# Kernel optimization log

Hardware: AMD Instinct MI355X
Metric: run time of the kernel (lower is better)

## Reference

```python
import jax, jax.numpy as jnp
import numpy as np

EPS = 0.5  # diffusion epsilon from init_kwargs

def setup_inputs() -> dict:
    key = jax.random.key(0)
    k = jax.random.split(key, 7)
    B, N0, N1, n = 1024, 32, 32, 64
    Mu0 = jax.random.normal(k[0], (N0, n), dtype=jnp.float32) * 2.0
    Mu1 = jax.random.normal(k[1], (N1, n), dtype=jnp.float32) * 2.0
    # diagonal covariances must be positive
    S0 = jax.random.uniform(k[2], (N0, n), dtype=jnp.float32, minval=0.1, maxval=1.0)
    S1 = jax.random.uniform(k[3], (N1, n), dtype=jnp.float32, minval=0.1, maxval=1.0)
    Lam = jax.random.uniform(k[4], (N0, N1), dtype=jnp.float32, minval=0.0, maxval=1.0)
    Lam = Lam / Lam.sum()  # transport plan sums to 1
    X = jax.random.normal(k[5], (B, n), dtype=jnp.float32)
    t = jnp.float32(0.3)
    return {"X": X, "Mu0": Mu0, "Mu1": Mu1, "S0": S0, "S1": S1, "Lam": Lam, "t": t}

def reference(X, Mu0, Mu1, S0, S1, Lam, t):
    eps2 = EPS * EPS
    S0e = S0[:, None, :]        # (N0,1,n)
    S1e = S1[None, :, :]        # (1,N1,n)
    Ds = jnp.sqrt(4.0 * S0e * S1e + EPS ** 4)
    Cs = 0.5 * (Ds - eps2)                       # (N0,N1,n)
    mu_t = (1.0 - t) * Mu0[:, None, :] + t * Mu1[None, :, :]  # (N0,N1,n)
    Sigma = (1.0 - t) ** 2 * S0e + t ** 2 * S1e + 2.0 * t * (1.0 - t) * (Cs + 0.5 * eps2)
    # St = Pt - Qt - eps^2 * t
    St = t * S1e + (1.0 - t) * Cs - ((1.0 - t) * S0e + t * Cs) - eps2 * t
    K = St / Sigma                               # (N0,N1,n)
    v = Mu1[None, :, :] - Mu0[:, None, :]        # (N0,N1,n)
    d = X[:, None, None, :] - mu_t               # (B,N0,N1,n)
    U = K * d + v                                # (B,N0,N1,n)
    # diag-Normal log_prob plus n/2*log(2pi) == -0.5*sum(d^2/Sigma + log Sigma)
    logw = -0.5 * jnp.sum(d * d / Sigma + jnp.log(Sigma), axis=-1)  # (B,N0,N1)
    W = jnp.exp(jnp.clip(logw, -50.0, 50.0)) * Lam                  # (B,N0,N1)
    num = jnp.einsum('bijn,bij->bn', U, W)       # (B,n)
    den = jnp.sum(W, axis=(1, 2))[:, None]       # (B,1)
    return num / den
```

## Files before the change

kernel.cpp:

```cpp
#include <hip/hip_runtime.h>
#include <math.h>

#define EPS2f 0.25f
#define EPS4f 0.0625f

__global__ __launch_bounds__(256) void precomp_kernel(
    const float* __restrict__ Mu0, const float* __restrict__ Mu1,
    const float* __restrict__ S0,  const float* __restrict__ S1,
    const float* __restrict__ tptr,
    float2* __restrict__ AB2, float2* __restrict__ KV2,
    float* __restrict__ C0)
{
    __shared__ float2 abS[4][67];
    __shared__ float2 kvS[4][64];

    const int tid = threadIdx.x;
    const int k   = tid & 63;
    const int ijl = tid >> 6;
    const int ij0 = blockIdx.x << 2;
    const int ij  = ij0 + ijl;
    const int i   = ij >> 5;
    const int j   = ij & 31;
    const float t   = *tptr;
    const float omt = 1.0f - t;

    const float s0 = S0[i * 64 + k];
    const float s1 = S1[j * 64 + k];
    const float m0 = Mu0[i * 64 + k];
    const float m1 = Mu1[j * 64 + k];

    const float ds  = sqrtf(4.0f * s0 * s1 + EPS4f);
    const float cs  = 0.5f * (ds - EPS2f);
    const float mt  = omt * m0 + t * m1;
    const float sig = omt * omt * s0 + t * t * s1
                    + 2.0f * t * omt * (cs + 0.5f * EPS2f);
    const float isig = 1.0f / sig;
    const float st = t * s1 - omt * s0 + (omt - t) * cs - EPS2f * t;
    const float kk = st * isig;
    const float v  = m1 - m0;

    abS[ijl][k] = make_float2(isig, 2.0f * mt * isig);
    kvS[ijl][k] = make_float2(kk, v - kk * mt);

    float c = mt * mt * isig + __logf(sig);
    #pragma unroll
    for (int off = 32; off >= 1; off >>= 1)
        c += __shfl_xor(c, off, 64);
    if (k == 0) C0[ij] = c;

    __syncthreads();

    {
        const int k2   = tid >> 3;
        const int ijl2 = (tid >> 1) & 3;
        const int par  = tid & 1;
        AB2[(k2 << 11) + ((ij0 + ijl2) << 1) + par] = abS[ijl2][2 * k2 + par];
    }
    {
        const int pr  = tid >> 7;
        const int k6  = (tid >> 1) & 63;
        const int par = tid & 1;
        KV2[(blockIdx.x << 8) + tid] = kvS[(pr << 1) + par][k6];
    }
}

__global__ __launch_bounds__(1024) void gmm_main_kernel(
    const float* __restrict__ X,   const float* __restrict__ Lam,
    const float* __restrict__ C0,
    const float4* __restrict__ AB4, const float4* __restrict__ KV4,
    float* __restrict__ out)
{
    __shared__ float4 Xs4[64];
    __shared__ float4 Wl4[1024 * 2];
    __shared__ float  red[16 * 64 * 5];
    __shared__ float  XsT[4 * 64];
    __shared__ float  denp[16 * 4];

    const int tid  = threadIdx.x;
    const int lane = tid & 63;
    const int w    = tid >> 6;
    const int b0   = blockIdx.x << 2;

    if (tid < 256) {
        const int bb = tid >> 6, k = tid & 63;
        const float xv = X[(b0 + bb) * 64 + k];
        ((float*)&Xs4[k])[bb] = xv;
        XsT[bb * 64 + k] = xv;
    }

    const int ij = tid;
    const float4* __restrict__ abp = AB4 + ij;
    const float c0 = C0[ij];
    const float lm = Lam[ij];

    float4 ab[8];
    #pragma unroll
    for (int g = 0; g < 8; ++g) ab[g] = abp[g << 10];

    __syncthreads();

    float qa = 0.f, qb = 0.f, qc = 0.f, qd = 0.f;
    #pragma unroll
    for (int k2 = 0; k2 < 32; ++k2) {
        const float4 a = ab[k2 & 7];
        if (k2 + 8 < 32) ab[k2 & 7] = abp[(k2 + 8) << 10];
        const float4 x0 = Xs4[2 * k2];
        const float4 x1 = Xs4[2 * k2 + 1];
        qa = fmaf(fmaf(a.x, x0.x, -a.y), x0.x, qa);
        qb = fmaf(fmaf(a.x, x0.y, -a.y), x0.y, qb);
        qc = fmaf(fmaf(a.x, x0.z, -a.y), x0.z, qc);
        qd = fmaf(fmaf(a.x, x0.w, -a.y), x0.w, qd);
        qa = fmaf(fmaf(a.z, x1.x, -a.w), x1.x, qa);
        qb = fmaf(fmaf(a.z, x1.y, -a.w), x1.y, qb);
        qc = fmaf(fmaf(a.z, x1.z, -a.w), x1.z, qc);
        qd = fmaf(fmaf(a.z, x1.w, -a.w), x1.w, qd);
    }

    #define WCALC(q) (__expf(fminf(fmaxf(-0.5f * ((q) + c0), -50.f), 50.f)) * lm)
    float4 wv4;
    wv4.x = WCALC(qa); wv4.y = WCALC(qb); wv4.z = WCALC(qc); wv4.w = WCALC(qd);
    #undef WCALC
    Wl4[ij * 2] = wv4;

    const int p0 = w << 5;
    float4 kvb[8];
    #pragma unroll
    for (int q = 0; q < 8; ++q) kvb[q] = KV4[((p0 + q) << 6) + lane];
    const float xk0 = XsT[0 * 64 + lane], xk1 = XsT[1 * 64 + lane];
    const float xk2 = XsT[2 * 64 + lane], xk3 = XsT[3 * 64 + lane];

    float d0 = wv4.x, d1 = wv4.y, d2 = wv4.z, d3 = wv4.w;
    #pragma unroll
    for (int off = 32; off >= 1; off >>= 1) {
        d0 += __shfl_xor(d0, off, 64);
        d1 += __shfl_xor(d1, off, 64);
        d2 += __shfl_xor(d2, off, 64);
        d3 += __shfl_xor(d3, off, 64);
    }
    if (lane == 0) {
        denp[w * 4 + 0] = d0; denp[w * 4 + 1] = d1;
        denp[w * 4 + 2] = d2; denp[w * 4 + 3] = d3;
    }

    float n0 = 0.f, n1 = 0.f, n2 = 0.f, n3 = 0.f;
    #pragma unroll
    for (int p = 0; p < 32; ++p) {
        const float4 kv = kvb[p & 7];
        if (p + 8 < 32) kvb[p & 7] = KV4[((p0 + p + 8) << 6) + lane];
        const float4 we = Wl4[(p0 + p) * 4];
        const float4 wo = Wl4[(p0 + p) * 4 + 2];
        float u;
        u = fmaf(kv.x, xk0, kv.y); n0 = fmaf(we.x, u, n0);
        u = fmaf(kv.x, xk1, kv.y); n1 = fmaf(we.y, u, n1);
        u = fmaf(kv.x, xk2, kv.y); n2 = fmaf(we.z, u, n2);
        u = fmaf(kv.x, xk3, kv.y); n3 = fmaf(we.w, u, n3);
        u = fmaf(kv.z, xk0, kv.w); n0 = fmaf(wo.x, u, n0);
        u = fmaf(kv.z, xk1, kv.w); n1 = fmaf(wo.y, u, n1);
        u = fmaf(kv.z, xk2, kv.w); n2 = fmaf(wo.z, u, n2);
        u = fmaf(kv.z, xk3, kv.w); n3 = fmaf(wo.w, u, n3);
    }
    {
        float* r = &red[(w * 64 + lane) * 5];
        r[0] = n0; r[1] = n1; r[2] = n2; r[3] = n3;
    }
    __syncthreads();

    if (tid < 256) {
        const int bb = tid >> 6, k = tid & 63;
        float s = 0.f, d = 0.f;
        #pragma unroll
        for (int ww = 0; ww < 16; ++ww) {
            s += red[(ww * 64 + k) * 5 + bb];
            d += denp[ww * 4 + bb];
        }
        out[(b0 + bb) * 64 + k] = s / d;
    }
}

extern "C" void kernel_launch(void* const* d_in, const int* in_sizes, int n_in,
                              void* d_out, int out_size, void* d_ws, size_t ws_size,
                              hipStream_t stream) {
    const float* X   = (const float*)d_in[0];
    const float* Mu0 = (const float*)d_in[1];
    const float* Mu1 = (const float*)d_in[2];
    const float* S0  = (const float*)d_in[3];
    const float* S1  = (const float*)d_in[4];
    const float* Lam = (const float*)d_in[5];
    const float* t   = (const float*)d_in[6];
    float* out = (float*)d_out;

    char* ws = (char*)d_ws;
    float2* AB2 = (float2*)(ws);
    float2* KV2 = (float2*)(ws + (512 << 10));
    float*  C0  = (float*)(ws + (1024 << 10));

    precomp_kernel<<<256, 256, 0, stream>>>(Mu0, Mu1, S0, S1, t, AB2, KV2, C0);
    gmm_main_kernel<<<256, 1024, 0, stream>>>(X, Lam, C0,
                                              (const float4*)AB2,
                                              (const float4*)KV2, out);
}
```

Baseline: 77.53 us.

## Fuse precompute and main kernels into one cooperative launch with grid sync

Merges the per-component precompute kernel into the main GMM kernel. The first 64 blocks compute the AB/KV/C0 tables and write them straight to global memory, without the shared-memory transpose, and a cooperative grid-wide sync separates that phase from the main computation. The aim is to remove the second kernel launch and the gap between the two kernels. In exchange it adds grid-sync overhead, scattered uncoalesced global writes, and a requirement that all 256 blocks of 1024 threads be co-resident.

```diff
diff --git a/kernel.cpp b/kernel.cpp
--- a/kernel.cpp
+++ b/kernel.cpp
@@ -1,80 +1,26 @@
 #include <hip/hip_runtime.h>
+#include <hip/hip_cooperative_groups.h>
 #include <math.h>
+
+namespace cg = cooperative_groups;
 
 #define EPS2f 0.25f
 #define EPS4f 0.0625f
 
-__global__ __launch_bounds__(256) void precomp_kernel(
-    const float* __restrict__ Mu0, const float* __restrict__ Mu1,
-    const float* __restrict__ S0,  const float* __restrict__ S1,
+__global__ __launch_bounds__(1024) void gmm_fused_kernel(
+    const float* __restrict__ X,   const float* __restrict__ Mu0,
+    const float* __restrict__ Mu1, const float* __restrict__ S0,
+    const float* __restrict__ S1,  const float* __restrict__ Lam,
     const float* __restrict__ tptr,
     float2* __restrict__ AB2, float2* __restrict__ KV2,
-    float* __restrict__ C0)
-{
-    __shared__ float2 abS[4][67];
-    __shared__ float2 kvS[4][64];
-
-    const int tid = threadIdx.x;
-    const int k   = tid & 63;
-    const int ijl = tid >> 6;
-    const int ij0 = blockIdx.x << 2;
-    const int ij  = ij0 + ijl;
-    const int i   = ij >> 5;
-    const int j   = ij & 31;
-    const float t   = *tptr;
-    const float omt = 1.0f - t;
-
-    const float s0 = S0[i * 64 + k];
-    const float s1 = S1[j * 64 + k];
-    const float m0 = Mu0[i * 64 + k];
-    const float m1 = Mu1[j * 64 + k];
-
-    const float ds  = sqrtf(4.0f * s0 * s1 + EPS4f);
-    const float cs  = 0.5f * (ds - EPS2f);
-    const float mt  = omt * m0 + t * m1;
-    const float sig = omt * omt * s0 + t * t * s1
-                    + 2.0f * t * omt * (cs + 0.5f * EPS2f);
-    const float isig = 1.0f / sig;
-    const float st = t * s1 - omt * s0 + (omt - t) * cs - EPS2f * t;
-    const float kk = st * isig;
-    const float v  = m1 - m0;
-
-    abS[ijl][k] = make_float2(isig, 2.0f * mt * isig);
-    kvS[ijl][k] = make_float2(kk, v - kk * mt);
-
-    float c = mt * mt * isig + __logf(sig);
-    #pragma unroll
-    for (int off = 32; off >= 1; off >>= 1)
-        c += __shfl_xor(c, off, 64);
-    if (k == 0) C0[ij] = c;
-
-    __syncthreads();
-
-    {
-        const int k2   = tid >> 3;
-        const int ijl2 = (tid >> 1) & 3;
-        const int par  = tid & 1;
-        AB2[(k2 << 11) + ((ij0 + ijl2) << 1) + par] = abS[ijl2][2 * k2 + par];
-    }
-    {
-        const int pr  = tid >> 7;
-        const int k6  = (tid >> 1) & 63;
-        const int par = tid & 1;
-        KV2[(blockIdx.x << 8) + tid] = kvS[(pr << 1) + par][k6];
-    }
-}
-
-__global__ __launch_bounds__(1024) void gmm_main_kernel(
-    const float* __restrict__ X,   const float* __restrict__ Lam,
-    const float* __restrict__ C0,
-    const float4* __restrict__ AB4, const float4* __restrict__ KV4,
+    float* __restrict__ C0,
     float* __restrict__ out)
 {
     __shared__ float4 Xs4[64];
     __shared__ float4 Wl4[1024 * 2];
     __shared__ float  red[16 * 64 * 5];
     __shared__ float  XsT[4 * 64];
-    __shared__ float  denp[16 * 4];
+    __shared__ float  denpS[16 * 4];
 
     const int tid  = threadIdx.x;
     const int lane = tid & 63;
@@ -88,6 +34,48 @@
         XsT[bb * 64 + k] = xv;
     }
 
+    if (blockIdx.x < 64) {
+        const int gid = (blockIdx.x << 10) + tid;
+        const int ij  = gid >> 6;
+        const int k   = gid & 63;
+        const int i   = ij >> 5;
+        const int j   = ij & 31;
+        const float t   = *tptr;
+        const float omt = 1.0f - t;
+
+        const float s0 = S0[i * 64 + k];
+        const float s1 = S1[j * 64 + k];
+        const float m0 = Mu0[i * 64 + k];
+        const float m1 = Mu1[j * 64 + k];
+
+        const float ds  = sqrtf(4.0f * s0 * s1 + EPS4f);
+        const float cs  = 0.5f * (ds - EPS2f);
+        const float mt  = omt * m0 + t * m1;
+        const float sig = omt * omt * s0 + t * t * s1
+                        + 2.0f * t * omt * (cs + 0.5f * EPS2f);
+        const float isig = 1.0f / sig;
+        const float st = t * s1 - omt * s0 + (omt - t) * cs - EPS2f * t;
+        const float kk = st * isig;
+        const float v  = m1 - m0;
+
+        AB2[((k >> 1) << 11) + (ij << 1) + (k & 1)] =
+            make_float2(isig, 2.0f * mt * isig);
+        KV2[((ij >> 1) << 7) + (k << 1) + (ij & 1)] =
+            make_float2(kk, v - kk * mt);
+
+        float c = mt * mt * isig + __logf(sig);
+        #pragma unroll
+        for (int off = 32; off >= 1; off >>= 1)
+            c += __shfl_xor(c, off, 64);
+        if (k == 0) C0[ij] = c;
+    }
+
+    __threadfence();
+    cg::this_grid().sync();
+
+    const float4* __restrict__ AB4 = (const float4*)AB2;
+    const float4* __restrict__ KV4 = (const float4*)KV2;
+
     const int ij = tid;
     const float4* __restrict__ abp = AB4 + ij;
     const float c0 = C0[ij];
@@ -96,8 +84,6 @@
     float4 ab[8];
     #pragma unroll
     for (int g = 0; g < 8; ++g) ab[g] = abp[g << 10];
-
-    __syncthreads();
 
     float qa = 0.f, qb = 0.f, qc = 0.f, qd = 0.f;
     #pragma unroll
@@ -138,8 +124,8 @@
         d3 += __shfl_xor(d3, off, 64);
     }
     if (lane == 0) {
-        denp[w * 4 + 0] = d0; denp[w * 4 + 1] = d1;
-        denp[w * 4 + 2] = d2; denp[w * 4 + 3] = d3;
+        denpS[w * 4 + 0] = d0; denpS[w * 4 + 1] = d1;
+        denpS[w * 4 + 2] = d2; denpS[w * 4 + 3] = d3;
     }
 
     float n0 = 0.f, n1 = 0.f, n2 = 0.f, n3 = 0.f;
@@ -171,7 +157,7 @@
         #pragma unroll
         for (int ww = 0; ww < 16; ++ww) {
             s += red[(ww * 64 + k) * 5 + bb];
-            d += denp[ww * 4 + bb];
+            d += denpS[ww * 4 + bb];
         }
         out[(b0 + bb) * 64 + k] = s / d;
     }
@@ -194,8 +180,9 @@
     float2* KV2 = (float2*)(ws + (512 << 10));
     float*  C0  = (float*)(ws + (1024 << 10));
 
-    precomp_kernel<<<256, 256, 0, stream>>>(Mu0, Mu1, S0, S1, t, AB2, KV2, C0);
-    gmm_main_kernel<<<256, 1024, 0, stream>>>(X, Lam, C0,
-                                              (const float4*)AB2,
-                                              (const float4*)KV2, out);
+    void* args[] = { (void*)&X, (void*)&Mu0, (void*)&Mu1, (void*)&S0,
+                     (void*)&S1, (void*)&Lam, (void*)&t,
+                     (void*)&AB2, (void*)&KV2, (void*)&C0, (void*)&out };
+    hipLaunchCooperativeKernel((const void*)gmm_fused_kernel,
+                               dim3(256), dim3(1024), args, 0, stream);
 }
```

After: 200.2 us. 158% more time.
